# Kernel optimization log

Measured on AMD Instinct MI355X. Metric: run time of the kernel, lower is better.

## Reference

```python
import jax, jax.numpy as jnp
import numpy as np

N = 50000        # nodes
E = 800000       # edges (edge-nodes of the line graph)
LGE = 1600000    # line-graph edges
F_NODE = 256     # node feature dim
T = 64           # timestamp/edge feature dim
HID = 128        # hidden size
OUT = 64         # out size
SLOPE = 0.2      # leaky relu negative slope used in EdgeGCN / attention


def _glorot(key, shape):
    lim = jnp.sqrt(6.0 / (shape[0] + shape[1]))
    return jax.random.uniform(key, shape, jnp.float32, -lim, lim)


def setup_inputs() -> dict:
    key = jax.random.key(0)
    ks = jax.random.split(key, 24)
    inp = {
        "x": jax.random.normal(ks[0], (N, F_NODE), jnp.float32),
        "et": jax.random.normal(ks[1], (E, T), jnp.float32),
        "H": jax.random.randint(ks[2], (2, E), 0, N),
        "raw_edge_index": jax.random.randint(ks[3], (2, E), 0, N),
        "lg_edge_index": jax.random.randint(ks[4], (2, LGE), 0, E),
        # TSAEncoder: two SAGE-style layers on the line graph (T->HID->HID)
        "W_tsa1_s": _glorot(ks[5], (T, HID)),
        "W_tsa1_n": _glorot(ks[6], (T, HID)),
        "W_tsa2_s": _glorot(ks[7], (HID, HID)),
        "W_tsa2_n": _glorot(ks[8], (HID, HID)),
        # EdgeToNodeConv + EdgeGCN output linear
        "W_etn": _glorot(ks[9], (HID, HID)),
        "W_eg_lin": _glorot(ks[10], (HID, HID)),
        # edge_aggr SAGE (num_layers-1 = 1 layer)
        "W_ea_s": _glorot(ks[11], (HID, HID)),
        "W_ea_n": _glorot(ks[12], (HID, HID)),
        # attr_node_model SAGE (2 layers)
        "W_an1_s": _glorot(ks[13], (F_NODE, HID)),
        "W_an1_n": _glorot(ks[14], (F_NODE, HID)),
        "W_an2_s": _glorot(ks[15], (HID, HID)),
        "W_an2_n": _glorot(ks[16], (HID, HID)),
        # MixAttention
        "Wq": _glorot(ks[17], (HID, HID)),
        "Wk": _glorot(ks[18], (HID, HID)),
        "Wv": _glorot(ks[19], (HID, HID)),
        # final classifier
        "W_out": _glorot(ks[20], (HID, OUT)),
    }
    return inp


def _sage(h, src, dst, Ws, Wn, n):
    # mean-aggregator SAGE conv: self transform + mean of in-neighbors
    deg = jnp.clip(jax.ops.segment_sum(jnp.ones(src.shape[0], h.dtype), dst, num_segments=n), 1.0)
    nbr = jax.ops.segment_sum(h[src], dst, num_segments=n) / deg[:, None]
    return h @ Ws + nbr @ Wn


def reference(x, et, H, raw_edge_index, lg_edge_index,
              W_tsa1_s, W_tsa1_n, W_tsa2_s, W_tsa2_n,
              W_etn, W_eg_lin, W_ea_s, W_ea_n,
              W_an1_s, W_an1_n, W_an2_s, W_an2_n,
              Wq, Wk, Wv, W_out):
    src_lg, dst_lg = lg_edge_index[0], lg_edge_index[1]
    src, dst = raw_edge_index[0], raw_edge_index[1]

    # ---- EdgeGCN: TSAEncoder over line graph (edges as nodes) ----
    h = jax.nn.relu(_sage(et, src_lg, dst_lg, W_tsa1_s, W_tsa1_n, E))
    h = _sage(h, src_lg, dst_lg, W_tsa2_s, W_tsa2_n, E)          # [E, HID]

    # ---- EdgeToNodeConv: scatter edge reprs to both incident nodes (mean) ----
    ones_e = jnp.ones(E, h.dtype)
    agg = (jax.ops.segment_sum(h, H[0], num_segments=N)
           + jax.ops.segment_sum(h, H[1], num_segments=N))        # [N, HID]
    deg = jnp.clip(jax.ops.segment_sum(ones_e, H[0], num_segments=N)
                   + jax.ops.segment_sum(ones_e, H[1], num_segments=N), 1.0)
    node_e = (agg / deg[:, None]) @ W_etn
    edge_repr = jax.nn.leaky_relu(node_e, negative_slope=SLOPE) @ W_eg_lin  # [N, HID]

    # ---- edge_aggr: 1-layer SAGE over raw graph ----
    aggr_edge = _sage(edge_repr, src, dst, W_ea_s, W_ea_n, N)     # [N, HID]

    # ---- attr_node_model: 2-layer SAGE ----
    hn = jax.nn.relu(_sage(x, src, dst, W_an1_s, W_an1_n, N))
    hn = _sage(hn, src, dst, W_an2_s, W_an2_n, N)                 # [N, HID]

    # ---- MixAttention: edge-indexed cross attention (node queries, edge-repr keys/values) ----
    q = hn @ Wq
    k = aggr_edge @ Wk
    v = aggr_edge @ Wv
    score = jax.nn.leaky_relu(
        jnp.sum(q[dst] * k[src], axis=-1) / jnp.sqrt(jnp.asarray(HID, q.dtype)),
        negative_slope=SLOPE)                                     # [E]
    m = jax.ops.segment_max(score, dst, num_segments=N)
    m = jnp.where(jnp.isfinite(m), m, 0.0)
    ex = jnp.exp(score - m[dst])
    den = jnp.clip(jax.ops.segment_sum(ex, dst, num_segments=N), 1e-9)
    alpha = ex / den[dst]
    out = hn + jax.ops.segment_sum(alpha[:, None] * v[src], dst, num_segments=N)

    return jax.nn.log_softmax(out @ W_out, axis=1)                # [N, OUT]
```

## Files before the change

kernel.cpp:

```cpp
#include <hip/hip_runtime.h>
#include <cstddef>

static constexpr int Nn   = 50000;
static constexpr int Ee   = 800000;
static constexpr int LGEe = 1600000;

typedef __attribute__((ext_vector_type(8))) short bf16x8;
typedef __attribute__((ext_vector_type(4))) float f32x4;

__device__ __forceinline__ float bf2f(unsigned int u16) {
  return __uint_as_float(u16 << 16);
}
__device__ __forceinline__ unsigned int f2bf(float f) {
  unsigned int u = __float_as_uint(f);
  u += 0x7fffu + ((u >> 16) & 1u);
  return u >> 16;
}

__global__ __launch_bounds__(256)
void k_count_direct(const int* __restrict__ idx, int* __restrict__ cnt, int n) {
  int i = blockIdx.x * 256 + threadIdx.x;
  if (i < n) atomicAdd(&cnt[idx[i]], 1);
}
__global__ __launch_bounds__(256)
void k_count_comp(const int* __restrict__ Hrow, const int* __restrict__ dlg,
                  int* __restrict__ cnt, int n) {
  int i = blockIdx.x * 256 + threadIdx.x;
  if (i < n) atomicAdd(&cnt[Hrow[dlg[i]]], 1);
}
__global__ __launch_bounds__(256)
void k_scan1(const int* __restrict__ in, int* __restrict__ out,
             int* __restrict__ bsum, int n) {
  __shared__ int sd[256];
  int tid = threadIdx.x;
  int base = blockIdx.x * 1024 + tid * 4;
  int4 v = {0, 0, 0, 0};
  if (base < n) v = *(const int4*)(in + base);
  int s = v.x + v.y + v.z + v.w;
  sd[tid] = s; __syncthreads();
  for (int off = 1; off < 256; off <<= 1) {
    int t_ = (tid >= off) ? sd[tid - off] : 0; __syncthreads();
    sd[tid] += t_; __syncthreads();
  }
  int excl = sd[tid] - s;
  if (base < n) {
    int4 o; o.x = excl; o.y = o.x + v.x; o.z = o.y + v.y; o.w = o.z + v.z;
    *(int4*)(out + base) = o;
  }
  if (tid == 255) bsum[blockIdx.x] = sd[255];
}
__global__ __launch_bounds__(1024)
void k_scan2(int* __restrict__ b, int nb) {
  __shared__ int sd[1024];
  int tid = threadIdx.x;
  int v = (tid < nb) ? b[tid] : 0;
  sd[tid] = v; __syncthreads();
  for (int off = 1; off < 1024; off <<= 1) {
    int t_ = (tid >= off) ? sd[tid - off] : 0; __syncthreads();
    sd[tid] += t_; __syncthreads();
  }
  if (tid < nb) b[tid] = sd[tid] - v;
}
__global__ __launch_bounds__(256)
void k_scan3(int* __restrict__ out, const int* __restrict__ bsum, int n, int total) {
  int i = blockIdx.x * 256 + threadIdx.x;
  if (i < n) out[i] += bsum[i >> 10];
  if (i == 0) out[n] = total;
}
__global__ __launch_bounds__(256)
void k_fillA(const int* __restrict__ dlg, const int* __restrict__ slg,
             const int* __restrict__ ptr, int* __restrict__ cur,
             int* __restrict__ ent, int n) {
  int m = blockIdx.x * 256 + threadIdx.x;
  if (m >= n) return;
  int d = dlg[m];
  int pos = ptr[d] + atomicAdd(&cur[d], 1);
  ent[pos] = slg[m];
}
__global__ __launch_bounds__(256)
void k_fillB(const int* __restrict__ Hrow, const int* __restrict__ dlg,
             const int* __restrict__ slg, const int* __restrict__ ptrA,
             const int* __restrict__ ptrB, int* __restrict__ cur,
             int* __restrict__ entS, float* __restrict__ entW, int n) {
  int m = blockIdx.x * 256 + threadIdx.x;
  if (m >= n) return;
  int d = dlg[m];
  int seg = Hrow[d];
  int pos = ptrB[seg] + atomicAdd(&cur[seg], 1);
  entS[pos] = slg[m];
  int la = ptrA[d + 1] - ptrA[d];
  entW[pos] = 1.0f / (float)max(la, 1);
}
__global__ __launch_bounds__(256)
void k_fillC(const int* __restrict__ Hrow, const int* __restrict__ ptr,
             int* __restrict__ cur, int* __restrict__ ent, int n) {
  int e = blockIdx.x * 256 + threadIdx.x;
  if (e >= n) return;
  int seg = Hrow[e];
  int pos = ptr[seg] + atomicAdd(&cur[seg], 1);
  ent[pos] = e;
}
__global__ __launch_bounds__(256)
void k_fillD(const int* __restrict__ dstA, const int* __restrict__ srcA,
             const int* __restrict__ ptr, int* __restrict__ cur,
             int* __restrict__ ent, int n) {
  int e = blockIdx.x * 256 + threadIdx.x;
  if (e >= n) return;
  int seg = dstA[e];
  int pos = ptr[seg] + atomicAdd(&cur[seg], 1);
  ent[pos] = srcA[e];
}
__global__ __launch_bounds__(256)
void k_rdeg(const int* __restrict__ ptr, float* __restrict__ r, int n) {
  int i = blockIdx.x * 256 + threadIdx.x;
  if (i < n) r[i] = 1.0f / fmaxf((float)(ptr[i + 1] - ptr[i]), 1.0f);
}

#define MG_SWEEP(WP, ACC)                                                       \
  {                                                                             \
    bf16x8 Bh[2][4], Bl[2][4];                                                  \
    _Pragma("unroll")                                                           \
    for (int np = 0; np < 2; ++np) {                                            \
      int n = (wv * 2 + np) * 16 + nrow;                                        \
      _Pragma("unroll")                                                         \
      for (int kc = 0; kc < 4; ++kc) {                                          \
        int kr0 = kh * 128 + kc * 32 + kg * 8;                                  \
        _Pragma("unroll")                                                       \
        for (int j = 0; j < 8; ++j) {                                           \
          float w = (WP)[(size_t)(kr0 + j) * 128 + n];                          \
          unsigned int hi = f2bf(w);                                            \
          float lo = w - bf2f(hi);                                              \
          Bh[np][kc][j] = (short)(unsigned short)hi;                            \
          Bl[np][kc][j] = (short)(unsigned short)f2bf(lo);                      \
        }                                                                       \
      }                                                                         \
    }                                                                           \
    _Pragma("unroll")                                                           \
    for (int kc = 0; kc < 4; ++kc) {                                            \
      _Pragma("unroll")                                                         \
      for (int m = 0; m < 4; ++m) {                                             \
        int ss = m * 16 + nrow;                                                 \
        int idx = ss * 128 + ((kc * 32 + kg * 8) ^ ((ss & 7) << 3));            \
        bf16x8 ah = *(const bf16x8*)(sAh + idx);                                \
        bf16x8 al = *(const bf16x8*)(sAl + idx);                                \
        _Pragma("unroll")                                                       \
        for (int np = 0; np < 2; ++np) {                                        \
          ACC[m][np] = __builtin_amdgcn_mfma_f32_16x16x32_bf16(ah, Bh[np][kc], ACC[m][np], 0, 0, 0); \
          ACC[m][np] = __builtin_amdgcn_mfma_f32_16x16x32_bf16(al, Bh[np][kc], ACC[m][np], 0, 0, 0); \
          ACC[m][np] = __builtin_amdgcn_mfma_f32_16x16x32_bf16(ah, Bl[np][kc], ACC[m][np], 0, 0, 0); \
        }                                                                       \
      }                                                                         \
    }                                                                           \
  }

template <int DUAL>
__global__ __launch_bounds__(256)
void k_mgemm(int M, const float* __restrict__ A, int K,
             const float* __restrict__ W1, const float* __restrict__ W2,
             const float* __restrict__ dgA, int reluA, int act,
             float* __restrict__ C1, float* __restrict__ C2, int beta1)
{
  __shared__ __align__(16) unsigned char smem[34816];
  unsigned short* sAh = (unsigned short*)smem;
  unsigned short* sAl = (unsigned short*)(smem + 16384);
  float* stage = (float*)smem;

  const int t = threadIdx.x, wv = t >> 6, lane = t & 63;
  const int tr = t >> 4, tc = t & 15;
  const int nrow = lane & 15, kg = lane >> 4;
  const int row0 = blockIdx.x * 64;

  f32x4 acc1[4][2], acc2[4][2];
  #pragma unroll
  for (int m = 0; m < 4; ++m)
    #pragma unroll
    for (int np = 0; np < 2; ++np) {
      acc1[m][np] = (f32x4){0.f, 0.f, 0.f, 0.f};
      if (DUAL) acc2[m][np] = (f32x4){0.f, 0.f, 0.f, 0.f};
    }

  const int nkh = K >> 7;
  #pragma unroll 1
  for (int kh = 0; kh < nkh; ++kh) {
    if (kh) __syncthreads();
    #pragma unroll
    for (int j = 0; j < 8; ++j) {
      int idx = t + j * 256;
      int r = idx >> 5, c4 = idx & 31;
      int gr = row0 + r; if (gr > M - 1) gr = M - 1;
      float4 va = *(const float4*)(A + (size_t)gr * K + kh * 128 + c4 * 4);
      if (reluA) {
        va.x = fmaxf(va.x, 0.f); va.y = fmaxf(va.y, 0.f);
        va.z = fmaxf(va.z, 0.f); va.w = fmaxf(va.w, 0.f);
      }
      if (dgA) {
        float sc = dgA[gr];
        va.x *= sc; va.y *= sc; va.z *= sc; va.w *= sc;
      }
      float v[4] = {va.x, va.y, va.z, va.w};
      unsigned int h[4], l[4];
      #pragma unroll
      for (int q = 0; q < 4; ++q) {
        h[q] = f2bf(v[q]);
        l[q] = f2bf(v[q] - bf2f(h[q]));
      }
      int bidx = r * 128 + ((c4 * 4) ^ ((r & 7) << 3));
      uint2 ph = {h[0] | (h[1] << 16), h[2] | (h[3] << 16)};
      uint2 pl = {l[0] | (l[1] << 16), l[2] | (l[3] << 16)};
      *(uint2*)(sAh + bidx) = ph;
      *(uint2*)(sAl + bidx) = pl;
    }
    __syncthreads();

    MG_SWEEP(W1, acc1);
    if (DUAL) MG_SWEEP(W2, acc2);
  }

  __syncthreads();
  #pragma unroll
  for (int m = 0; m < 4; ++m)
    #pragma unroll
    for (int np = 0; np < 2; ++np)
      #pragma unroll
      for (int r = 0; r < 4; ++r)
        stage[(m * 16 + kg * 4 + r) * 132 + (wv * 2 + np) * 16 + nrow] = acc1[m][np][r];
  __syncthreads();
  #pragma unroll
  for (int i = 0; i < 4; ++i) {
    int s = tr * 4 + i, gr = row0 + s;
    if (gr >= M) continue;
    const float* sp = stage + s * 132 + tc * 8;
    float4 v0 = *(const float4*)sp, v1 = *(const float4*)(sp + 4);
    float o[8] = {v0.x, v0.y, v0.z, v0.w, v1.x, v1.y, v1.z, v1.w};
    #pragma unroll
    for (int j2 = 0; j2 < 8; ++j2) {
      float vv = o[j2];
      if (act == 1)      vv = fmaxf(vv, 0.f);
      else if (act == 2) vv = vv > 0.f ? vv : 0.2f * vv;
      o[j2] = vv;
    }
    float* p = C1 + (size_t)gr * 128 + tc * 8;
    if (beta1) {
      float4 c0 = *(const float4*)p, c1 = *(const float4*)(p + 4);
      o[0] += c0.x; o[1] += c0.y; o[2] += c0.z; o[3] += c0.w;
      o[4] += c1.x; o[5] += c1.y; o[6] += c1.z; o[7] += c1.w;
    }
    *(float4*)p       = *(const float4*)&o[0];
    *(float4*)(p + 4) = *(const float4*)&o[4];
  }
  if (DUAL) {
    __syncthreads();
    #pragma unroll
    for (int m = 0; m < 4; ++m)
      #pragma unroll
      for (int np = 0; np < 2; ++np)
        #pragma unroll
        for (int r = 0; r < 4; ++r)
          stage[(m * 16 + kg * 4 + r) * 132 + (wv * 2 + np) * 16 + nrow] = acc2[m][np][r];
    __syncthreads();
    #pragma unroll
    for (int i = 0; i < 4; ++i) {
      int s = tr * 4 + i, gr = row0 + s;
      if (gr >= M) continue;
      const float* sp = stage + s * 132 + tc * 8;
      float4 v0 = *(const float4*)sp, v1 = *(const float4*)(sp + 4);
      float o[8] = {v0.x, v0.y, v0.z, v0.w, v1.x, v1.y, v1.z, v1.w};
      #pragma unroll
      for (int j2 = 0; j2 < 8; ++j2) {
        float vv = o[j2];
        if (act == 1)      vv = fmaxf(vv, 0.f);
        else if (act == 2) vv = vv > 0.f ? vv : 0.2f * vv;
        o[j2] = vv;
      }
      float* p = C2 + (size_t)gr * 128 + tc * 8;
      *(float4*)p       = *(const float4*)&o[0];
      *(float4*)(p + 4) = *(const float4*)&o[4];
    }
  }
}

__global__ __launch_bounds__(256)
void k_tsa1(const float* __restrict__ et,
            const int* __restrict__ rp, const int* __restrict__ ent,
            const float* __restrict__ Ws, const float* __restrict__ Wn,
            unsigned short* __restrict__ BUF)
{
  __shared__ __align__(16) unsigned char smem[34816];
  unsigned short* sAh = (unsigned short*)smem;
  unsigned short* sAl = (unsigned short*)(smem + 16384);
  int*   sEnt  = (int*)(smem + 32768);
  float* stage = (float*)smem;

  const int t = threadIdx.x, wv = t >> 6, lane = t & 63;
  const int tr = t >> 4, tc = t & 15;
  const int nrow = lane & 15, kg = lane >> 4;
  const int seg0 = blockIdx.x * 64;
  const int segbase = seg0 + wv * 16;

  int rpv = (lane <= 16) ? rp[segbase + lane] : 0;
  int nxtv = __shfl(rpv, (lane + 1) & 63);
  float invv = 1.f / fmaxf((float)(nxtv - rpv), 1.f);

  const int base = rp[seg0];
  const int cnt  = rp[seg0 + 64] - base;
  const int lim  = cnt < 512 ? cnt : 512;
  for (int i = t; i < lim; i += 256) sEnt[i] = ent[base + i];

  {
    float dv[16];
    #pragma unroll
    for (int i = 0; i < 16; ++i)
      dv[i] = et[(size_t)(segbase + i) * 64 + lane];
    #pragma unroll
    for (int i = 0; i < 16; ++i) {
      int ss = wv * 16 + i;
      unsigned int hi = f2bf(dv[i]);
      float lo = dv[i] - bf2f(hi);
      int idx = ss * 128 + (lane ^ ((ss & 7) << 3));
      sAh[idx] = (unsigned short)hi;
      sAl[idx] = (unsigned short)f2bf(lo);
    }
  }

  bf16x8 Bh[2][4], Bl[2][4];
  #pragma unroll
  for (int np = 0; np < 2; ++np) {
    int n = (wv * 2 + np) * 16 + nrow;
    #pragma unroll
    for (int kc = 0; kc < 4; ++kc) {
      const float* Wp = (kc < 2) ? Ws : Wn;
      int kr0 = (kc & 1) * 32 + kg * 8;
      #pragma unroll
      for (int j = 0; j < 8; ++j) {
        float w = Wp[(size_t)(kr0 + j) * 128 + n];
        unsigned int hi = f2bf(w);
        float lo = w - bf2f(hi);
        Bh[np][kc][j] = (short)(unsigned short)hi;
        Bl[np][kc][j] = (short)(unsigned short)f2bf(lo);
      }
    }
  }
  __syncthreads();

  {
    int q0 = __shfl(rpv, 0);
    int q1 = __shfl(rpv, 16);
    int c = 0;
    int b_next = __shfl(rpv, 1);
    float idg = __shfl(invv, 0);
    float a = 0.f;
    #pragma unroll 1
    for (int j = q0; j < q1; j += 8) {
      float x[8];
      #pragma unroll
      for (int u = 0; u < 8; ++u) {
        int jj = j + u; jj = jj < q1 ? jj : q1 - 1;
        int ix = jj - base;
        int s = (ix < 512) ? sEnt[ix] : ent[jj];
        x[u] = et[(size_t)s * 64 + lane];
      }
      #pragma unroll
      for (int u = 0; u < 8; ++u) {
        int jj = j + u;
        if (jj >= q1) break;
        while (jj >= b_next) {
          float v = a * idg;
          int ss = wv * 16 + c;
          unsigned int hi = f2bf(v);
          float lo = v - bf2f(hi);
          int idx = ss * 128 + ((64 + lane) ^ ((ss & 7) << 3));
          sAh[idx] = (unsigned short)hi;
          sAl[idx] = (unsigned short)f2bf(lo);
          a = 0.f;
          ++c;
          b_next = __shfl(rpv, c + 1);
          idg = __shfl(invv, c);
        }
        a += x[u];
      }
    }
    #pragma unroll 1
    for (;;) {
      float v = a * idg;
      int ss = wv * 16 + c;
      unsigned int hi = f2bf(v);
      float lo = v - bf2f(hi);
      int idx = ss * 128 + ((64 + lane) ^ ((ss & 7) << 3));
      sAh[idx] = (unsigned short)hi;
      sAl[idx] = (unsigned short)f2bf(lo);
      a = 0.f;
      if (++c >= 16) break;
      idg = __shfl(invv, c);
    }
  }
  __syncthreads();

  f32x4 acc[4][2];
  #pragma unroll
  for (int m = 0; m < 4; ++m)
    #pragma unroll
    for (int np = 0; np < 2; ++np)
      acc[m][np] = (f32x4){0.f, 0.f, 0.f, 0.f};

  #pragma unroll
  for (int kc = 0; kc < 4; ++kc) {
    #pragma unroll
    for (int m = 0; m < 4; ++m) {
      int ss = m * 16 + nrow;
      int kbase = kc * 32 + kg * 8;
      int idx = ss * 128 + (kbase ^ ((ss & 7) << 3));
      bf16x8 ah = *(const bf16x8*)(sAh + idx);
      bf16x8 al = *(const bf16x8*)(sAl + idx);
      #pragma unroll
      for (int np = 0; np < 2; ++np) {
        acc[m][np] = __builtin_amdgcn_mfma_f32_16x16x32_bf16(ah, Bh[np][kc], acc[m][np], 0, 0, 0);
        acc[m][np] = __builtin_amdgcn_mfma_f32_16x16x32_bf16(al, Bh[np][kc], acc[m][np], 0, 0, 0);
        acc[m][np] = __builtin_amdgcn_mfma_f32_16x16x32_bf16(ah, Bl[np][kc], acc[m][np], 0, 0, 0);
      }
    }
  }

  __syncthreads();
  #pragma unroll
  for (int m = 0; m < 4; ++m)
    #pragma unroll
    for (int np = 0; np < 2; ++np)
      #pragma unroll
      for (int r = 0; r < 4; ++r)
        stage[(m * 16 + kg * 4 + r) * 132 + (wv * 2 + np) * 16 + nrow] = acc[m][np][r];
  __syncthreads();
  #pragma unroll
  for (int i = 0; i < 4; ++i) {
    int s = tr * 4 + i;
    const float* sp = stage + s * 132 + tc * 8;
    float4 v0 = *(const float4*)sp;
    float4 v1 = *(const float4*)(sp + 4);
    unsigned int pk[4];
    pk[0] = f2bf(v0.x) | (f2bf(v0.y) << 16);
    pk[1] = f2bf(v0.z) | (f2bf(v0.w) << 16);
    pk[2] = f2bf(v1.x) | (f2bf(v1.y) << 16);
    pk[3] = f2bf(v1.z) | (f2bf(v1.w) << 16);
    uint4 st = {pk[0], pk[1], pk[2], pk[3]};
    *(uint4*)(BUF + (size_t)(seg0 + s) * 128 + tc * 8) = st;
  }
}

__global__ __launch_bounds__(256)
void k_poolb(const int* __restrict__ rp, const int* __restrict__ ent,
             const float* __restrict__ entw,
             const unsigned short* __restrict__ SRC,
             float* __restrict__ O, int nseg, int total)
{
  const int wv = threadIdx.x >> 6, lane = threadIdx.x & 63;
  const int chunk = blockIdx.x * 4 + wv;
  const int c0 = chunk * 256;
  if (c0 >= total) return;
  int c1 = c0 + 256; if (c1 > total) c1 = total;

  int lo = 0, hi = nseg;
  while (lo + 1 < hi) {
    int mid = (lo + hi) >> 1;
    if (rp[mid] <= c0) lo = mid; else hi = mid;
  }
  int seg = lo;
  int sstart = rp[seg];
  int send = rp[seg + 1];
  float a0 = 0.f, a1 = 0.f;

  #pragma unroll 1
  for (int j = c0; j < c1; j += 8) {
    int ids[8]; float w[8];
    #pragma unroll
    for (int u = 0; u < 8; ++u) {
      int jj = j + u; jj = jj < c1 ? jj : c1 - 1;
      ids[u] = ent[jj];
      w[u] = entw ? entw[jj] : 1.f;
    }
    unsigned int uv[8];
    #pragma unroll
    for (int u = 0; u < 8; ++u)
      uv[u] = *(const unsigned int*)(SRC + (size_t)ids[u] * 128 + 2 * lane);
    #pragma unroll
    for (int u = 0; u < 8; ++u) {
      int jj = j + u;
      if (jj >= c1) break;
      while (jj >= send) {
        float* p = O + (size_t)seg * 128;
        if (sstart >= c0 && send <= c1) {
          p[2 * lane]     += a0;
          p[2 * lane + 1] += a1;
        } else {
          atomicAdd(p + 2 * lane, a0);
          atomicAdd(p + 2 * lane + 1, a1);
        }
        a0 = a1 = 0.f;
        ++seg; sstart = send; send = rp[seg + 1];
      }
      a0 = fmaf(w[u], fmaxf(bf2f(uv[u] & 0xffffu), 0.f), a0);
      a1 = fmaf(w[u], fmaxf(bf2f(uv[u] >> 16),     0.f), a1);
    }
  }
  {
    float* p = O + (size_t)seg * 128;
    if (sstart >= c0 && send <= c1) {
      p[2 * lane]     += a0;
      p[2 * lane + 1] += a1;
    } else {
      atomicAdd(p + 2 * lane, a0);
      atomicAdd(p + 2 * lane + 1, a1);
    }
  }
}

__global__ __launch_bounds__(256)
void k_poolf(const int* __restrict__ rp, const int* __restrict__ ent,
             const float* __restrict__ SRC, float* __restrict__ O,
             int nseg, int total)
{
  const int wv = threadIdx.x >> 6, lane = threadIdx.x & 63;
  const int chunk = blockIdx.x * 4 + wv;
  const int c0 = chunk * 256;
  if (c0 >= total) return;
  int c1 = c0 + 256; if (c1 > total) c1 = total;

  int lo = 0, hi = nseg;
  while (lo + 1 < hi) {
    int mid = (lo + hi) >> 1;
    if (rp[mid] <= c0) lo = mid; else hi = mid;
  }
  int seg = lo;
  int sstart = rp[seg];
  int send = rp[seg + 1];
  float a0 = 0.f, a1 = 0.f;

  #pragma unroll 1
  for (int j = c0; j < c1; j += 8) {
    int ids[8];
    #pragma unroll
    for (int u = 0; u < 8; ++u) {
      int jj = j + u; jj = jj < c1 ? jj : c1 - 1;
      ids[u] = ent[jj];
    }
    float2 v[8];
    #pragma unroll
    for (int u = 0; u < 8; ++u)
      v[u] = ((const float2*)(SRC + (size_t)ids[u] * 128))[lane];
    #pragma unroll
    for (int u = 0; u < 8; ++u) {
      int jj = j + u;
      if (jj >= c1) break;
      while (jj >= send) {
        float sc = 1.f / fmaxf((float)(send - sstart), 1.f);
        float* p = O + (size_t)seg * 128;
        if (sstart >= c0 && send <= c1) {
          p[2 * lane]     += a0 * sc;
          p[2 * lane + 1] += a1 * sc;
        } else {
          atomicAdd(p + 2 * lane, a0 * sc);
          atomicAdd(p + 2 * lane + 1, a1 * sc);
        }
        a0 = a1 = 0.f;
        ++seg; sstart = send; send = rp[seg + 1];
      }
      a0 += v[u].x; a1 += v[u].y;
    }
  }
  {
    float sc = 1.f / fmaxf((float)(send - sstart), 1.f);
    float* p = O + (size_t)seg * 128;
    if (sstart >= c0 && send <= c1) {
      p[2 * lane]     += a0 * sc;
      p[2 * lane + 1] += a1 * sc;
    } else {
      atomicAdd(p + 2 * lane, a0 * sc);
      atomicAdd(p + 2 * lane + 1, a1 * sc);
    }
  }
}

__global__ __launch_bounds__(256)
void k_attn(const int* __restrict__ rp, const int* __restrict__ ent,
            const float* __restrict__ q, const float* __restrict__ kb,
            const float* __restrict__ vb, float* __restrict__ o, int nseg)
{
  int wv = threadIdx.x >> 6, lane = threadIdx.x & 63;
  int seg = blockIdx.x * 4 + wv;
  if (seg >= nseg) return;
  int p0 = rp[seg], p1 = rp[seg + 1];
  if (p0 >= p1) return;
  float2 q2 = ((const float2*)(q + (size_t)seg * 128))[lane];
  float m = -1e30f, l = 0.f, o0 = 0.f, o1 = 0.f;
  #pragma unroll 1
  for (int j = p0; j < p1; j += 4) {
    int s[4];
    #pragma unroll
    for (int i = 0; i < 4; ++i) {
      int jj = j + i; jj = jj < p1 ? jj : p1 - 1;
      s[i] = ent[jj];
    }
    float2 k2[4], v2[4];
    #pragma unroll
    for (int i = 0; i < 4; ++i)
      k2[i] = ((const float2*)(kb + (size_t)s[i] * 128))[lane];
    #pragma unroll
    for (int i = 0; i < 4; ++i)
      v2[i] = ((const float2*)(vb + (size_t)s[i] * 128))[lane];
    float d[4];
    #pragma unroll
    for (int i = 0; i < 4; ++i) d[i] = fmaf(q2.x, k2[i].x, q2.y * k2[i].y);
    #pragma unroll
    for (int off = 1; off < 64; off <<= 1) {
      #pragma unroll
      for (int i = 0; i < 4; ++i) d[i] += __shfl_xor(d[i], off);
    }
    float sc[4];
    #pragma unroll
    for (int i = 0; i < 4; ++i) {
      float v = d[i] * 0.088388347648318447f;
      v = v > 0.f ? v : 0.2f * v;
      sc[i] = (j + i < p1) ? v : -1e30f;
    }
    float mb = fmaxf(fmaxf(sc[0], sc[1]), fmaxf(sc[2], sc[3]));
    float mn = fmaxf(m, mb);
    float scale = expf(m - mn);
    float e[4];
    #pragma unroll
    for (int i = 0; i < 4; ++i)
      e[i] = (j + i < p1) ? expf(sc[i] - mn) : 0.f;
    l  = l  * scale + ((e[0] + e[1]) + (e[2] + e[3]));
    o0 = o0 * scale + ((e[0] * v2[0].x + e[1] * v2[1].x) + (e[2] * v2[2].x + e[3] * v2[3].x));
    o1 = o1 * scale + ((e[0] * v2[0].y + e[1] * v2[1].y) + (e[2] * v2[2].y + e[3] * v2[3].y));
    m = mn;
  }
  float inv = 1.f / fmaxf(l, 1e-9f);
  float2* orow = (float2*)(o + (size_t)seg * 128);
  float2 cur = orow[lane];
  cur.x += o0 * inv; cur.y += o1 * inv;
  orow[lane] = cur;
}

__global__ __launch_bounds__(256)
void k_out(const float* __restrict__ attn, const float* __restrict__ Wout,
           float* __restrict__ out, int n) {
  __shared__ float sW[128 * 64];
  for (int i = threadIdx.x; i < 128 * 64; i += 256) sW[i] = Wout[i];
  __syncthreads();
  int wave = threadIdx.x >> 6, lane = threadIdx.x & 63;
  int row = blockIdx.x * 4 + wave;
  if (row >= n) return;
  const float* a = attn + (size_t)row * 128;
  float z = 0.f;
  #pragma unroll 8
  for (int k = 0; k < 128; ++k) z = fmaf(a[k], sW[k * 64 + lane], z);
  float mx = z;
  #pragma unroll
  for (int off = 32; off; off >>= 1) mx = fmaxf(mx, __shfl_xor(mx, off));
  float ee = expf(z - mx);
  float ss = ee;
  #pragma unroll
  for (int off = 32; off; off >>= 1) ss += __shfl_xor(ss, off);
  out[(size_t)row * 64 + lane] = z - mx - logf(ss);
}

extern "C" void kernel_launch(void* const* d_in, const int* in_sizes, int n_in,
                              void* d_out, int out_size, void* d_ws, size_t ws_size,
                              hipStream_t stream) {
  (void)in_sizes; (void)n_in; (void)out_size;
  const float* x        = (const float*)d_in[0];
  const float* et       = (const float*)d_in[1];
  const int*   H0       = (const int*)d_in[2];
  const int*   H1       = H0 + Ee;
  const int*   src      = (const int*)d_in[3];
  const int*   dst      = src + Ee;
  const int*   src_lg   = (const int*)d_in[4];
  const int*   dst_lg   = src_lg + LGEe;
  const float* W_tsa1_s = (const float*)d_in[5];
  const float* W_tsa1_n = (const float*)d_in[6];
  const float* W_tsa2_s = (const float*)d_in[7];
  const float* W_tsa2_n = (const float*)d_in[8];
  const float* W_etn    = (const float*)d_in[9];
  const float* W_eg_lin = (const float*)d_in[10];
  const float* W_ea_s   = (const float*)d_in[11];
  const float* W_ea_n   = (const float*)d_in[12];
  const float* W_an1_s  = (const float*)d_in[13];
  const float* W_an1_n  = (const float*)d_in[14];
  const float* W_an2_s  = (const float*)d_in[15];
  const float* W_an2_n  = (const float*)d_in[16];
  const float* Wq       = (const float*)d_in[17];
  const float* Wk       = (const float*)d_in[18];
  const float* Wv       = (const float*)d_in[19];
  const float* W_out    = (const float*)d_in[20];
  float* out = (float*)d_out;

  char* wp = (char*)d_ws;
  size_t avail = ws_size;
  auto alloc = [&](size_t bytes) -> void* {
    void* r = (void*)wp;
    size_t pad = (bytes + 255) & ~(size_t)255;
    wp += pad; avail = (avail >= pad) ? avail - pad : 0;
    return r;
  };
  const size_t NH = (size_t)Nn * 128;
  unsigned short* BUF = (unsigned short*)alloc((size_t)Ee * 128 * 2);
  float* agg   = (float*)alloc(NH * 4);
  int* ptrA  = (int*)alloc(((size_t)Ee + 1) * 4);
  int* cntA  = (int*)alloc((size_t)Ee * 4);
  int* entA  = (int*)alloc((size_t)LGEe * 4);
  int* ptrB  = (int*)alloc(((size_t)Nn + 1) * 4);
  int* cntB  = (int*)alloc((size_t)Nn * 4);
  int* entBs = (int*)alloc((size_t)2 * LGEe * 4);
  float* entBw = (float*)alloc((size_t)2 * LGEe * 4);
  int* ptrC  = (int*)alloc(((size_t)Nn + 1) * 4);
  int* cntC  = (int*)alloc((size_t)Nn * 4);
  int* entC  = (int*)alloc((size_t)2 * Ee * 4);
  int* ptrD  = (int*)alloc(((size_t)Nn + 1) * 4);
  int* cntD  = (int*)alloc((size_t)Nn * 4);
  int* entD  = (int*)alloc((size_t)Ee * 4);
  float* rdegN = (float*)alloc((size_t)Nn * 4);
  int* bsum  = (int*)alloc(2048 * 4);
  if (avail == 0 && wp > (char*)d_ws + ws_size) return;

  float* er  = (float*)BUF + 0 * NH;
  float* ae  = (float*)BUF + 1 * NH;
  float* hn  = (float*)BUF + 2 * NH;
  float* hn2 = (float*)BUF + 3 * NH;
  float* qb  = (float*)BUF + 4 * NH;
  float* kb  = (float*)BUF + 5 * NH;
  float* vb  = (float*)BUF + 6 * NH;
  float* tmp = (float*)BUF + 7 * NH;
  float* T = (float*)entBs;

  auto cdiv = [](long a, long b) { return (int)((a + b - 1) / b); };
  auto scan = [&](int* cnt, int* ptr, int n, int total) {
    int nb = cdiv(n, 1024);
    k_scan1<<<nb, 256, 0, stream>>>(cnt, ptr, bsum, n);
    k_scan2<<<1, 1024, 0, stream>>>(bsum, nb);
    k_scan3<<<cdiv(n, 256), 256, 0, stream>>>(ptr, bsum, n, total);
  };

  const int gLG = cdiv(LGEe, 256), gEe = cdiv(Ee, 256);

  hipMemsetAsync(cntA, 0, (size_t)Ee * 4, stream);
  k_count_direct<<<gLG, 256, 0, stream>>>(dst_lg, cntA, LGEe);
  scan(cntA, ptrA, Ee, LGEe);
  hipMemsetAsync(cntA, 0, (size_t)Ee * 4, stream);
  k_fillA<<<gLG, 256, 0, stream>>>(dst_lg, src_lg, ptrA, cntA, entA, LGEe);

  hipMemsetAsync(cntB, 0, (size_t)Nn * 4, stream);
  k_count_comp<<<gLG, 256, 0, stream>>>(H0, dst_lg, cntB, LGEe);
  k_count_comp<<<gLG, 256, 0, stream>>>(H1, dst_lg, cntB, LGEe);
  scan(cntB, ptrB, Nn, 2 * LGEe);
  hipMemsetAsync(cntB, 0, (size_t)Nn * 4, stream);
  k_fillB<<<gLG, 256, 0, stream>>>(H0, dst_lg, src_lg, ptrA, ptrB, cntB, entBs, entBw, LGEe);
  k_fillB<<<gLG, 256, 0, stream>>>(H1, dst_lg, src_lg, ptrA, ptrB, cntB, entBs, entBw, LGEe);

  hipMemsetAsync(cntC, 0, (size_t)Nn * 4, stream);
  k_count_direct<<<gEe, 256, 0, stream>>>(H0, cntC, Ee);
  k_count_direct<<<gEe, 256, 0, stream>>>(H1, cntC, Ee);
  scan(cntC, ptrC, Nn, 2 * Ee);
  hipMemsetAsync(cntC, 0, (size_t)Nn * 4, stream);
  k_fillC<<<gEe, 256, 0, stream>>>(H0, ptrC, cntC, entC, Ee);
  k_fillC<<<gEe, 256, 0, stream>>>(H1, ptrC, cntC, entC, Ee);

  hipMemsetAsync(cntD, 0, (size_t)Nn * 4, stream);
  k_count_direct<<<gEe, 256, 0, stream>>>(dst, cntD, Ee);
  scan(cntD, ptrD, Nn, Ee);
  hipMemsetAsync(cntD, 0, (size_t)Nn * 4, stream);
  k_fillD<<<gEe, 256, 0, stream>>>(dst, src, ptrD, cntD, entD, Ee);
  k_rdeg<<<cdiv(Nn, 256), 256, 0, stream>>>(ptrC, rdegN, Nn);

  const int gM64  = cdiv(Nn, 64);
  const int gW    = cdiv(Nn, 4);
  const int gP2   = cdiv(cdiv(2 * LGEe, 256), 4);
  const int gP1   = cdiv(cdiv(2 * Ee, 256), 4);
  const int gPf   = cdiv(cdiv(Ee, 256), 4);

  k_tsa1<<<Ee / 64, 256, 0, stream>>>(et, ptrA, entA, W_tsa1_s, W_tsa1_n, BUF);

  hipMemsetAsync(agg, 0, NH * 4, stream);
  k_poolb<<<gP2, 256, 0, stream>>>(ptrB, entBs, entBw, BUF, agg, Nn, 2 * LGEe);
  k_mgemm<0><<<gM64, 256, 0, stream>>>(Nn, agg, 128, W_tsa2_n, nullptr, nullptr, 0, 0, T, nullptr, 0);
  hipMemsetAsync(agg, 0, NH * 4, stream);
  k_poolb<<<gP1, 256, 0, stream>>>(ptrC, entC, nullptr, BUF, agg, Nn, 2 * Ee);
  k_mgemm<0><<<gM64, 256, 0, stream>>>(Nn, agg, 128, W_tsa2_s, nullptr, nullptr, 0, 0, T, nullptr, 1);
  k_mgemm<0><<<gM64, 256, 0, stream>>>(Nn, T, 128, W_etn, nullptr, rdegN, 0, 2, tmp, nullptr, 0);
  k_mgemm<0><<<gM64, 256, 0, stream>>>(Nn, tmp, 128, W_eg_lin, nullptr, nullptr, 0, 0, er, nullptr, 0);

  k_mgemm<1><<<gM64, 256, 0, stream>>>(Nn, er, 128, W_ea_s, W_ea_n, nullptr, 0, 0, ae, tmp, 0);
  k_poolf<<<gPf, 256, 0, stream>>>(ptrD, entD, tmp, ae, Nn, Ee);

  k_mgemm<1><<<gM64, 256, 0, stream>>>(Nn, x, 256, W_an1_s, W_an1_n, nullptr, 0, 0, hn, tmp, 0);
  k_poolf<<<gPf, 256, 0, stream>>>(ptrD, entD, tmp, hn, Nn, Ee);
  k_mgemm<1><<<gM64, 256, 0, stream>>>(Nn, hn, 128, W_an2_s, W_an2_n, nullptr, 1, 0, hn2, tmp, 0);
  k_poolf<<<gPf, 256, 0, stream>>>(ptrD, entD, tmp, hn2, Nn, Ee);

  k_mgemm<0><<<gM64, 256, 0, stream>>>(Nn, hn2, 128, Wq, nullptr, nullptr, 0, 0, qb, nullptr, 0);
  k_mgemm<1><<<gM64, 256, 0, stream>>>(Nn, ae, 128, Wk, Wv, nullptr, 0, 0, kb, vb, 0);
  k_attn<<<gW, 256, 0, stream>>>(ptrD, entD, qb, kb, vb, hn2, Nn);

  k_out<<<gW, 256, 0, stream>>>(hn2, W_out, out, Nn);
}
```

Before: 2.302 ms.

## Fuse line-graph neighbor pooling into node pooling and drop composed CSR build

Removes the composed node-to-line-graph CSR (count, scan and two fill passes over the line-graph edges). A new pooling kernel walks the node-to-edge CSR and, for each edge, gathers its line-graph neighbors through the edge CSR on the fly. It accumulates the self sum and the degree-normalised neighbor sum into two buffers in one pass. The scan now writes the fill cursors directly, which removes memsets and pointer reads in the fill kernels, and the H0/H1 count and fill launches are merged into single launches. The bf16 hi/lo split switches from round-to-nearest to truncation, which costs fewer instructions but slightly enlarges the rounding error, and the nested variable-length inner loop may cause wave divergence.

```diff
diff --git a/kernel.cpp b/kernel.cpp
--- a/kernel.cpp
+++ b/kernel.cpp
@@ -21,12 +21,6 @@
 void k_count_direct(const int* __restrict__ idx, int* __restrict__ cnt, int n) {
   int i = blockIdx.x * 256 + threadIdx.x;
   if (i < n) atomicAdd(&cnt[idx[i]], 1);
-}
-__global__ __launch_bounds__(256)
-void k_count_comp(const int* __restrict__ Hrow, const int* __restrict__ dlg,
-                  int* __restrict__ cnt, int n) {
-  int i = blockIdx.x * 256 + threadIdx.x;
-  if (i < n) atomicAdd(&cnt[Hrow[dlg[i]]], 1);
 }
 __global__ __launch_bounds__(256)
 void k_scan1(const int* __restrict__ in, int* __restrict__ out,
@@ -62,52 +56,38 @@
   if (tid < nb) b[tid] = sd[tid] - v;
 }
 __global__ __launch_bounds__(256)
-void k_scan3(int* __restrict__ out, const int* __restrict__ bsum, int n, int total) {
+void k_scan3(int* __restrict__ out, const int* __restrict__ bsum, int n, int total,
+             int* __restrict__ cur) {
   int i = blockIdx.x * 256 + threadIdx.x;
-  if (i < n) out[i] += bsum[i >> 10];
+  if (i < n) {
+    int v = out[i] + bsum[i >> 10];
+    out[i] = v;
+    cur[i] = v;
+  }
   if (i == 0) out[n] = total;
 }
 __global__ __launch_bounds__(256)
 void k_fillA(const int* __restrict__ dlg, const int* __restrict__ slg,
-             const int* __restrict__ ptr, int* __restrict__ cur,
-             int* __restrict__ ent, int n) {
+             int* __restrict__ cur, int* __restrict__ ent, int n) {
   int m = blockIdx.x * 256 + threadIdx.x;
   if (m >= n) return;
-  int d = dlg[m];
-  int pos = ptr[d] + atomicAdd(&cur[d], 1);
+  int pos = atomicAdd(&cur[dlg[m]], 1);
   ent[pos] = slg[m];
 }
 __global__ __launch_bounds__(256)
-void k_fillB(const int* __restrict__ Hrow, const int* __restrict__ dlg,
-             const int* __restrict__ slg, const int* __restrict__ ptrA,
-             const int* __restrict__ ptrB, int* __restrict__ cur,
-             int* __restrict__ entS, float* __restrict__ entW, int n) {
-  int m = blockIdx.x * 256 + threadIdx.x;
-  if (m >= n) return;
-  int d = dlg[m];
-  int seg = Hrow[d];
-  int pos = ptrB[seg] + atomicAdd(&cur[seg], 1);
-  entS[pos] = slg[m];
-  int la = ptrA[d + 1] - ptrA[d];
-  entW[pos] = 1.0f / (float)max(la, 1);
-}
-__global__ __launch_bounds__(256)
-void k_fillC(const int* __restrict__ Hrow, const int* __restrict__ ptr,
+void k_fillC2(const int* __restrict__ H, int* __restrict__ cur,
+              int* __restrict__ ent, int n2, int E) {
+  int i = blockIdx.x * 256 + threadIdx.x;
+  if (i >= n2) return;
+  int pos = atomicAdd(&cur[H[i]], 1);
+  ent[pos] = (i >= E) ? i - E : i;
+}
+__global__ __launch_bounds__(256)
+void k_fillD(const int* __restrict__ dstA, const int* __restrict__ srcA,
              int* __restrict__ cur, int* __restrict__ ent, int n) {
   int e = blockIdx.x * 256 + threadIdx.x;
   if (e >= n) return;
-  int seg = Hrow[e];
-  int pos = ptr[seg] + atomicAdd(&cur[seg], 1);
-  ent[pos] = e;
-}
-__global__ __launch_bounds__(256)
-void k_fillD(const int* __restrict__ dstA, const int* __restrict__ srcA,
-             const int* __restrict__ ptr, int* __restrict__ cur,
-             int* __restrict__ ent, int n) {
-  int e = blockIdx.x * 256 + threadIdx.x;
-  if (e >= n) return;
-  int seg = dstA[e];
-  int pos = ptr[seg] + atomicAdd(&cur[seg], 1);
+  int pos = atomicAdd(&cur[dstA[e]], 1);
   ent[pos] = srcA[e];
 }
 __global__ __launch_bounds__(256)
@@ -128,10 +108,10 @@
         _Pragma("unroll")                                                       \
         for (int j = 0; j < 8; ++j) {                                           \
           float w = (WP)[(size_t)(kr0 + j) * 128 + n];                          \
-          unsigned int hi = f2bf(w);                                            \
+          unsigned int hi = __float_as_uint(w) >> 16;                           \
           float lo = w - bf2f(hi);                                              \
           Bh[np][kc][j] = (short)(unsigned short)hi;                            \
-          Bl[np][kc][j] = (short)(unsigned short)f2bf(lo);                      \
+          Bl[np][kc][j] = (short)(unsigned short)(__float_as_uint(lo) >> 16);   \
         }                                                                       \
       }                                                                         \
     }                                                                           \
@@ -165,9 +145,9 @@
   unsigned short* sAl = (unsigned short*)(smem + 16384);
   float* stage = (float*)smem;
 
-  const int t = threadIdx.x, wv = t >> 6, lane = t & 63;
+  const int t = threadIdx.x, wv = t >> 6;
   const int tr = t >> 4, tc = t & 15;
-  const int nrow = lane & 15, kg = lane >> 4;
+  const int nrow = (t & 63) & 15, kg = (t & 63) >> 4;
   const int row0 = blockIdx.x * 64;
 
   f32x4 acc1[4][2], acc2[4][2];
@@ -201,8 +181,8 @@
       unsigned int h[4], l[4];
       #pragma unroll
       for (int q = 0; q < 4; ++q) {
-        h[q] = f2bf(v[q]);
-        l[q] = f2bf(v[q] - bf2f(h[q]));
+        h[q] = __float_as_uint(v[q]) >> 16;
+        l[q] = __float_as_uint(v[q] - bf2f(h[q])) >> 16;
       }
       int bidx = r * 128 + ((c4 * 4) ^ ((r & 7) << 3));
       uint2 ph = {h[0] | (h[1] << 16), h[2] | (h[3] << 16)};
@@ -314,11 +294,11 @@
     #pragma unroll
     for (int i = 0; i < 16; ++i) {
       int ss = wv * 16 + i;
-      unsigned int hi = f2bf(dv[i]);
+      unsigned int hi = __float_as_uint(dv[i]) >> 16;
       float lo = dv[i] - bf2f(hi);
       int idx = ss * 128 + (lane ^ ((ss & 7) << 3));
       sAh[idx] = (unsigned short)hi;
-      sAl[idx] = (unsigned short)f2bf(lo);
+      sAl[idx] = (unsigned short)(__float_as_uint(lo) >> 16);
     }
   }
 
@@ -333,10 +313,10 @@
       #pragma unroll
       for (int j = 0; j < 8; ++j) {
         float w = Wp[(size_t)(kr0 + j) * 128 + n];
-        unsigned int hi = f2bf(w);
+        unsigned int hi = __float_as_uint(w) >> 16;
         float lo = w - bf2f(hi);
         Bh[np][kc][j] = (short)(unsigned short)hi;
-        Bl[np][kc][j] = (short)(unsigned short)f2bf(lo);
+        Bl[np][kc][j] = (short)(unsigned short)(__float_as_uint(lo) >> 16);
       }
     }
   }
@@ -366,11 +346,11 @@
         while (jj >= b_next) {
           float v = a * idg;
           int ss = wv * 16 + c;
-          unsigned int hi = f2bf(v);
+          unsigned int hi = __float_as_uint(v) >> 16;
           float lo = v - bf2f(hi);
           int idx = ss * 128 + ((64 + lane) ^ ((ss & 7) << 3));
           sAh[idx] = (unsigned short)hi;
-          sAl[idx] = (unsigned short)f2bf(lo);
+          sAl[idx] = (unsigned short)(__float_as_uint(lo) >> 16);
           a = 0.f;
           ++c;
           b_next = __shfl(rpv, c + 1);
@@ -383,11 +363,11 @@
     for (;;) {
       float v = a * idg;
       int ss = wv * 16 + c;
-      unsigned int hi = f2bf(v);
+      unsigned int hi = __float_as_uint(v) >> 16;
       float lo = v - bf2f(hi);
       int idx = ss * 128 + ((64 + lane) ^ ((ss & 7) << 3));
       sAh[idx] = (unsigned short)hi;
-      sAl[idx] = (unsigned short)f2bf(lo);
+      sAl[idx] = (unsigned short)(__float_as_uint(lo) >> 16);
       a = 0.f;
       if (++c >= 16) break;
       idg = __shfl(invv, c);
@@ -446,16 +426,17 @@
 }
 
 __global__ __launch_bounds__(256)
-void k_poolb(const int* __restrict__ rp, const int* __restrict__ ent,
-             const float* __restrict__ entw,
-             const unsigned short* __restrict__ SRC,
-             float* __restrict__ O, int nseg, int total)
+void k_pool12(const int* __restrict__ rp, const int* __restrict__ ent,
+              const int* __restrict__ rpA, const int* __restrict__ entA,
+              const unsigned short* __restrict__ BUF,
+              float* __restrict__ OS, float* __restrict__ ON,
+              int nseg, int total)
 {
   const int wv = threadIdx.x >> 6, lane = threadIdx.x & 63;
   const int chunk = blockIdx.x * 4 + wv;
-  const int c0 = chunk * 256;
+  const int c0 = chunk * 128;
   if (c0 >= total) return;
-  int c1 = c0 + 256; if (c1 > total) c1 = total;
+  int c1 = c0 + 128; if (c1 > total) c1 = total;
 
   int lo = 0, hi = nseg;
   while (lo + 1 < hi) {
@@ -465,49 +446,72 @@
   int seg = lo;
   int sstart = rp[seg];
   int send = rp[seg + 1];
-  float a0 = 0.f, a1 = 0.f;
+  float s0 = 0.f, s1 = 0.f, n0 = 0.f, n1 = 0.f;
 
   #pragma unroll 1
   for (int j = c0; j < c1; j += 8) {
-    int ids[8]; float w[8];
+    int ids[8];
     #pragma unroll
     for (int u = 0; u < 8; ++u) {
       int jj = j + u; jj = jj < c1 ? jj : c1 - 1;
       ids[u] = ent[jj];
-      w[u] = entw ? entw[jj] : 1.f;
     }
     unsigned int uv[8];
+    int pA0[8], pA1[8];
     #pragma unroll
     for (int u = 0; u < 8; ++u)
-      uv[u] = *(const unsigned int*)(SRC + (size_t)ids[u] * 128 + 2 * lane);
+      uv[u] = *(const unsigned int*)(BUF + (size_t)ids[u] * 128 + 2 * lane);
+    #pragma unroll
+    for (int u = 0; u < 8; ++u) { pA0[u] = rpA[ids[u]]; pA1[u] = rpA[ids[u] + 1]; }
     #pragma unroll
     for (int u = 0; u < 8; ++u) {
       int jj = j + u;
       if (jj >= c1) break;
       while (jj >= send) {
-        float* p = O + (size_t)seg * 128;
+        float* pS = OS + (size_t)seg * 128;
+        float* pN = ON + (size_t)seg * 128;
         if (sstart >= c0 && send <= c1) {
-          p[2 * lane]     += a0;
-          p[2 * lane + 1] += a1;
+          pS[2 * lane]     += s0;  pS[2 * lane + 1] += s1;
+          pN[2 * lane]     += n0;  pN[2 * lane + 1] += n1;
         } else {
-          atomicAdd(p + 2 * lane, a0);
-          atomicAdd(p + 2 * lane + 1, a1);
+          atomicAdd(pS + 2 * lane, s0);     atomicAdd(pS + 2 * lane + 1, s1);
+          atomicAdd(pN + 2 * lane, n0);     atomicAdd(pN + 2 * lane + 1, n1);
         }
-        a0 = a1 = 0.f;
+        s0 = s1 = n0 = n1 = 0.f;
         ++seg; sstart = send; send = rp[seg + 1];
       }
-      a0 = fmaf(w[u], fmaxf(bf2f(uv[u] & 0xffffu), 0.f), a0);
-      a1 = fmaf(w[u], fmaxf(bf2f(uv[u] >> 16),     0.f), a1);
+      s0 += fmaxf(bf2f(uv[u] & 0xffffu), 0.f);
+      s1 += fmaxf(bf2f(uv[u] >> 16),     0.f);
+      int p0 = pA0[u], p1 = pA1[u];
+      float a0 = 0.f, a1 = 0.f;
+      #pragma unroll 1
+      for (int t2 = p0; t2 < p1; t2 += 4) {
+        unsigned int w[4];
+        int rem = p1 - t2;
+        #pragma unroll
+        for (int v2 = 0; v2 < 4; ++v2)
+          if (v2 < rem)
+            w[v2] = *(const unsigned int*)(BUF + (size_t)entA[t2 + v2] * 128 + 2 * lane);
+        #pragma unroll
+        for (int v2 = 0; v2 < 4; ++v2)
+          if (v2 < rem) {
+            a0 += fmaxf(bf2f(w[v2] & 0xffffu), 0.f);
+            a1 += fmaxf(bf2f(w[v2] >> 16),     0.f);
+          }
+      }
+      float idg = 1.f / fmaxf((float)(p1 - p0), 1.f);
+      n0 += a0 * idg; n1 += a1 * idg;
     }
   }
   {
-    float* p = O + (size_t)seg * 128;
+    float* pS = OS + (size_t)seg * 128;
+    float* pN = ON + (size_t)seg * 128;
     if (sstart >= c0 && send <= c1) {
-      p[2 * lane]     += a0;
-      p[2 * lane + 1] += a1;
+      pS[2 * lane]     += s0;  pS[2 * lane + 1] += s1;
+      pN[2 * lane]     += n0;  pN[2 * lane + 1] += n1;
     } else {
-      atomicAdd(p + 2 * lane, a0);
-      atomicAdd(p + 2 * lane + 1, a1);
+      atomicAdd(pS + 2 * lane, s0);     atomicAdd(pS + 2 * lane + 1, s1);
+      atomicAdd(pN + 2 * lane, n0);     atomicAdd(pN + 2 * lane + 1, n1);
     }
   }
 }
@@ -669,7 +673,6 @@
   const float* x        = (const float*)d_in[0];
   const float* et       = (const float*)d_in[1];
   const int*   H0       = (const int*)d_in[2];
-  const int*   H1       = H0 + Ee;
   const int*   src      = (const int*)d_in[3];
   const int*   dst      = src + Ee;
   const int*   src_lg   = (const int*)d_in[4];
@@ -702,14 +705,11 @@
   };
   const size_t NH = (size_t)Nn * 128;
   unsigned short* BUF = (unsigned short*)alloc((size_t)Ee * 128 * 2);
-  float* agg   = (float*)alloc(NH * 4);
+  float* aggN  = (float*)alloc(NH * 4);
+  float* aggS  = (float*)alloc(NH * 4);
   int* ptrA  = (int*)alloc(((size_t)Ee + 1) * 4);
   int* cntA  = (int*)alloc((size_t)Ee * 4);
   int* entA  = (int*)alloc((size_t)LGEe * 4);
-  int* ptrB  = (int*)alloc(((size_t)Nn + 1) * 4);
-  int* cntB  = (int*)alloc((size_t)Nn * 4);
-  int* entBs = (int*)alloc((size_t)2 * LGEe * 4);
-  float* entBw = (float*)alloc((size_t)2 * LGEe * 4);
   int* ptrC  = (int*)alloc(((size_t)Nn + 1) * 4);
   int* cntC  = (int*)alloc((size_t)Nn * 4);
   int* entC  = (int*)alloc((size_t)2 * Ee * 4);
@@ -728,62 +728,46 @@
   float* kb  = (float*)BUF + 5 * NH;
   float* vb  = (float*)BUF + 6 * NH;
   float* tmp = (float*)BUF + 7 * NH;
-  float* T = (float*)entBs;
 
   auto cdiv = [](long a, long b) { return (int)((a + b - 1) / b); };
   auto scan = [&](int* cnt, int* ptr, int n, int total) {
     int nb = cdiv(n, 1024);
     k_scan1<<<nb, 256, 0, stream>>>(cnt, ptr, bsum, n);
     k_scan2<<<1, 1024, 0, stream>>>(bsum, nb);
-    k_scan3<<<cdiv(n, 256), 256, 0, stream>>>(ptr, bsum, n, total);
+    k_scan3<<<cdiv(n, 256), 256, 0, stream>>>(ptr, bsum, n, total, cnt);
   };
 
-  const int gLG = cdiv(LGEe, 256), gEe = cdiv(Ee, 256);
+  const int gLG = cdiv(LGEe, 256), gEe = cdiv(Ee, 256), g2E = cdiv(2 * Ee, 256);
 
   hipMemsetAsync(cntA, 0, (size_t)Ee * 4, stream);
   k_count_direct<<<gLG, 256, 0, stream>>>(dst_lg, cntA, LGEe);
   scan(cntA, ptrA, Ee, LGEe);
-  hipMemsetAsync(cntA, 0, (size_t)Ee * 4, stream);
-  k_fillA<<<gLG, 256, 0, stream>>>(dst_lg, src_lg, ptrA, cntA, entA, LGEe);
-
-  hipMemsetAsync(cntB, 0, (size_t)Nn * 4, stream);
-  k_count_comp<<<gLG, 256, 0, stream>>>(H0, dst_lg, cntB, LGEe);
-  k_count_comp<<<gLG, 256, 0, stream>>>(H1, dst_lg, cntB, LGEe);
-  scan(cntB, ptrB, Nn, 2 * LGEe);
-  hipMemsetAsync(cntB, 0, (size_t)Nn * 4, stream);
-  k_fillB<<<gLG, 256, 0, stream>>>(H0, dst_lg, src_lg, ptrA, ptrB, cntB, entBs, entBw, LGEe);
-  k_fillB<<<gLG, 256, 0, stream>>>(H1, dst_lg, src_lg, ptrA, ptrB, cntB, entBs, entBw, LGEe);
+  k_fillA<<<gLG, 256, 0, stream>>>(dst_lg, src_lg, cntA, entA, LGEe);
 
   hipMemsetAsync(cntC, 0, (size_t)Nn * 4, stream);
-  k_count_direct<<<gEe, 256, 0, stream>>>(H0, cntC, Ee);
-  k_count_direct<<<gEe, 256, 0, stream>>>(H1, cntC, Ee);
+  k_count_direct<<<g2E, 256, 0, stream>>>(H0, cntC, 2 * Ee);
   scan(cntC, ptrC, Nn, 2 * Ee);
-  hipMemsetAsync(cntC, 0, (size_t)Nn * 4, stream);
-  k_fillC<<<gEe, 256, 0, stream>>>(H0, ptrC, cntC, entC, Ee);
-  k_fillC<<<gEe, 256, 0, stream>>>(H1, ptrC, cntC, entC, Ee);
+  k_fillC2<<<g2E, 256, 0, stream>>>(H0, cntC, entC, 2 * Ee, Ee);
 
   hipMemsetAsync(cntD, 0, (size_t)Nn * 4, stream);
   k_count_direct<<<gEe, 256, 0, stream>>>(dst, cntD, Ee);
   scan(cntD, ptrD, Nn, Ee);
-  hipMemsetAsync(cntD, 0, (size_t)Nn * 4, stream);
-  k_fillD<<<gEe, 256, 0, stream>>>(dst, src, ptrD, cntD, entD, Ee);
+  k_fillD<<<gEe, 256, 0, stream>>>(dst, src, cntD, entD, Ee);
   k_rdeg<<<cdiv(Nn, 256), 256, 0, stream>>>(ptrC, rdegN, Nn);
 
   const int gM64  = cdiv(Nn, 64);
   const int gW    = cdiv(Nn, 4);
-  const int gP2   = cdiv(cdiv(2 * LGEe, 256), 4);
-  const int gP1   = cdiv(cdiv(2 * Ee, 256), 4);
+  const int gP12  = cdiv(cdiv(2 * Ee, 128), 4);
   const int gPf   = cdiv(cdiv(Ee, 256), 4);
 
   k_tsa1<<<Ee / 64, 256, 0, stream>>>(et, ptrA, entA, W_tsa1_s, W_tsa1_n, BUF);
 
-  hipMemsetAsync(agg, 0, NH * 4, stream);
-  k_poolb<<<gP2, 256, 0, stream>>>(ptrB, entBs, entBw, BUF, agg, Nn, 2 * LGEe);
-  k_mgemm<0><<<gM64, 256, 0, stream>>>(Nn, agg, 128, W_tsa2_n, nullptr, nullptr, 0, 0, T, nullptr, 0);
-  hipMemsetAsync(agg, 0, NH * 4, stream);
-  k_poolb<<<gP1, 256, 0, stream>>>(ptrC, entC, nullptr, BUF, agg, Nn, 2 * Ee);
-  k_mgemm<0><<<gM64, 256, 0, stream>>>(Nn, agg, 128, W_tsa2_s, nullptr, nullptr, 0, 0, T, nullptr, 1);
-  k_mgemm<0><<<gM64, 256, 0, stream>>>(Nn, T, 128, W_etn, nullptr, rdegN, 0, 2, tmp, nullptr, 0);
+  hipMemsetAsync(aggS, 0, NH * 4, stream);
+  hipMemsetAsync(aggN, 0, NH * 4, stream);
+  k_pool12<<<gP12, 256, 0, stream>>>(ptrC, entC, ptrA, entA, BUF, aggS, aggN, Nn, 2 * Ee);
+  k_mgemm<0><<<gM64, 256, 0, stream>>>(Nn, aggN, 128, W_tsa2_n, nullptr, nullptr, 0, 0, aggN, nullptr, 0);
+  k_mgemm<0><<<gM64, 256, 0, stream>>>(Nn, aggS, 128, W_tsa2_s, nullptr, nullptr, 0, 0, aggN, nullptr, 1);
+  k_mgemm<0><<<gM64, 256, 0, stream>>>(Nn, aggN, 128, W_etn, nullptr, rdegN, 0, 2, tmp, nullptr, 0);
   k_mgemm<0><<<gM64, 256, 0, stream>>>(Nn, tmp, 128, W_eg_lin, nullptr, nullptr, 0, 0, er, nullptr, 0);
 
   k_mgemm<1><<<gM64, 256, 0, stream>>>(Nn, er, 128, W_ea_s, W_ea_n, nullptr, 0, 0, ae, tmp, 0);
```

After: 2.356 ms. +2.3%, slower.
